# Optimization experiments

Hardware: AMD Instinct MI355X
Metric: run time of the kernel (lower is better)

Reference implementation:

```python
import jax, jax.numpy as jnp
import numpy as np

jax.config.update("jax_enable_x64", True)  # exact int64 fixed-point requantization

QMIN, QMAX = 0, 255  # 8-bit asymmetric activations


def _mul_m0_shift(acc, M0, shift):
    """gemmlowp-style fixed-point rescale: round((acc*M0)>>31) >> shift (rounding)."""
    prod = acc.astype(jnp.int64) * M0.astype(jnp.int64)
    nudge = jnp.where(prod >= 0, jnp.int64(1 << 30), jnp.int64(1 - (1 << 30)))
    hi = (prod + nudge) >> 31  # rounding-doubling high mul
    sh = shift.astype(jnp.int64)
    return (hi + (jnp.int64(1) << (sh - 1))) >> sh  # rounding right shift


def _requant(acc, M0, shift, z_out):
    return jnp.clip(_mul_m0_shift(acc, M0, shift) + z_out, QMIN, QMAX).astype(jnp.int32)


def _qconv(q, w, z_in, M0, shift, z_out, pad):
    # int8-style conv: subtract input zero-point, integer accumulate (exact in fp32
    # since |acc| < 2^24 by construction), then fixed-point requantize.
    xf = (q - z_in).astype(jnp.float32)
    acc = jax.lax.conv_general_dilated(
        xf, w, (1, 1), [(pad, pad), (pad, pad)],
        dimension_numbers=("NCHW", "OIHW", "NCHW"))
    return _requant(jnp.round(acc).astype(jnp.int64), M0, shift, z_out)


def _qbn(q, z_in, w, b, M0, shift, z_out):
    # fused quantized BN: per-channel integer affine + fixed-point requantize
    acc = (q.astype(jnp.int64) - z_in) * w.astype(jnp.int64)[None, :, None, None] \
          + b.astype(jnp.int64)[None, :, None, None]
    return _requant(acc, M0, shift, z_out)


def setup_inputs() -> dict:
    key = jax.random.key(0)
    ks = jax.random.split(key, 10)
    B, Cin, H, W = 32, 256, 56, 56
    width, Cout = 64, 256
    x = jax.random.randint(ks[0], (B, Cin, H, W), 0, 256, dtype=jnp.int32)
    w1 = jax.random.randint(ks[1], (width, Cin, 1, 1), -63, 64).astype(jnp.float32)
    w2 = jax.random.randint(ks[2], (width, width, 3, 3), -63, 64).astype(jnp.float32)
    w3 = jax.random.randint(ks[3], (Cout, width, 1, 1), -63, 64).astype(jnp.float32)
    bn1_w = jax.random.randint(ks[4], (width,), 100, 160).astype(jnp.float32)
    bn1_b = jax.random.randint(ks[5], (width,), -1000, 1000).astype(jnp.float32)
    bn2_w = jax.random.randint(ks[6], (width,), 100, 160).astype(jnp.float32)
    bn2_b = jax.random.randint(ks[7], (width,), -1000, 1000).astype(jnp.float32)
    bn3_w = jax.random.randint(ks[8], (Cout,), 100, 160).astype(jnp.float32)
    bn3_b = jax.random.randint(ks[9], (Cout,), -1000, 1000).astype(jnp.float32)
    conv_zin = jnp.array([128, 128, 128], jnp.int32)
    conv_m0 = jnp.array([1518500250] * 3, jnp.int32)
    conv_shift = jnp.array([9, 9, 9], jnp.int32)
    conv_zout = jnp.array([128, 128, 128], jnp.int32)
    bn_m0 = jnp.array([1073741824] * 3, jnp.int32)
    bn_shift = jnp.array([6, 6, 6], jnp.int32)
    bn_zout = jnp.array([128, 128, 128], jnp.int32)
    add_z = jnp.array([128, 128], jnp.int32)
    add_m0 = jnp.array([1073741824] * 2, jnp.int32)
    add_shift = jnp.array([1, 1], jnp.int32)
    add_zout = jnp.array(128, jnp.int32)
    return dict(x=x, w1=w1, w2=w2, w3=w3,
                bn1_w=bn1_w, bn1_b=bn1_b, bn2_w=bn2_w, bn2_b=bn2_b,
                bn3_w=bn3_w, bn3_b=bn3_b,
                conv_zin=conv_zin, conv_m0=conv_m0, conv_shift=conv_shift,
                conv_zout=conv_zout, bn_m0=bn_m0, bn_shift=bn_shift,
                bn_zout=bn_zout, add_z=add_z, add_m0=add_m0,
                add_shift=add_shift, add_zout=add_zout)


def reference(x, w1, w2, w3, bn1_w, bn1_b, bn2_w, bn2_b, bn3_w, bn3_b,
              conv_zin, conv_m0, conv_shift, conv_zout,
              bn_m0, bn_shift, bn_zout,
              add_z, add_m0, add_shift, add_zout):
    identity = x  # a_bit == target_bit -> rescale_matrix path skipped, conv_x = x
    out = _qconv(x, w1, conv_zin[0], conv_m0[0], conv_shift[0], conv_zout[0], 0)
    out = _qbn(out, conv_zout[0], bn1_w, bn1_b, bn_m0[0], bn_shift[0], bn_zout[0])
    out = _qconv(out, w2, conv_zin[1], conv_m0[1], conv_shift[1], conv_zout[1], 1)
    out = _qbn(out, conv_zout[1], bn2_w, bn2_b, bn_m0[1], bn_shift[1], bn_zout[1])
    out = _qconv(out, w3, conv_zin[2], conv_m0[2], conv_shift[2], conv_zout[2], 0)
    out = _qbn(out, conv_zout[2], bn3_w, bn3_b, bn_m0[2], bn_shift[2], bn_zout[2])
    # QuantizedAdd: rescale both branches to the output scale, add, clamp
    ra = _mul_m0_shift(identity.astype(jnp.int64) - add_z[0], add_m0[0], add_shift[0])
    rb = _mul_m0_shift(out.astype(jnp.int64) - add_z[1], add_m0[1], add_shift[1])
    return jnp.clip(ra + rb + add_zout, QMIN, QMAX).astype(jnp.int32)
```

## Files before the change

### kernel.cpp

```cpp
#include <hip/hip_runtime.h>


typedef int v4i __attribute__((ext_vector_type(4)));

#define BATCH 32
#define CIN 256
#define CMID 64
#define HW 3136
#define W56 56

__device__ __forceinline__ int requant_q(int acc, int M0, int shift, int zout) {
    long long prod = (long long)acc * (long long)M0;
    long long nudge = (prod >= 0) ? (1LL << 30) : (1LL - (1LL << 30));
    long long hi = (prod + nudge) >> 31;
    long long r = (hi + (1LL << (shift - 1))) >> shift;
    int v = (int)r + zout;
    return v < 0 ? 0 : (v > 255 ? 255 : v);
}

__device__ __forceinline__ long long mulshift_ll(long long v, int M0, int shift) {
    long long prod = v * (long long)M0;
    long long nudge = (prod >= 0) ? (1LL << 30) : (1LL - (1LL << 30));
    long long hi = (prod + nudge) >> 31;
    return (hi + (1LL << (shift - 1))) >> shift;
}

__device__ __forceinline__ v4i pack16f(const float* src, int stride) {
    v4i r;
#pragma unroll
    for (int d = 0; d < 4; ++d) {
        unsigned int u = 0;
#pragma unroll
        for (int by = 0; by < 4; ++by) {
            int v = (int)src[(d * 4 + by) * stride];
            u |= ((unsigned int)(v & 255)) << (8 * by);
        }
        r[d] = (int)u;
    }
    return r;
}

__global__ __launch_bounds__(256) void k_conv1(
    const int* __restrict__ x, const float* __restrict__ w1,
    const float* __restrict__ bn_w, const float* __restrict__ bn_b,
    const int* __restrict__ conv_zin, const int* __restrict__ conv_m0,
    const int* __restrict__ conv_shift, const int* __restrict__ conv_zout,
    const int* __restrict__ bn_m0, const int* __restrict__ bn_shift,
    const int* __restrict__ bn_zout, signed char* __restrict__ t1)
{
    __shared__ v4i sm[640];
    const int tid = threadIdx.x, lane = tid & 63, wv = tid >> 6;
    const int col = lane & 15, koff = lane >> 4;
    const int nbase = blockIdx.x * 128;
    const int co0 = wv * 16;

    v4i a[4];
#pragma unroll
    for (int ks = 0; ks < 4; ++ks)
        a[ks] = pack16f(w1 + (size_t)(co0 + col) * 256 + ks * 64 + koff * 16, 1);

    const int p = tid & 127, ch = tid >> 7;
    const int np = nbase + p;
    const int pb = np / HW, phw = np - pb * HW;
    const int zin = conv_zin[0];

    v4i acc[8];
#pragma unroll
    for (int i = 0; i < 8; ++i) acc[i] = (v4i){0, 0, 0, 0};

    for (int ks = 0; ks < 4; ++ks) {
        unsigned int pk[8];
        const size_t xb = ((size_t)pb * CIN + ks * 64 + ch * 32) * HW + phw;
#pragma unroll
        for (int d = 0; d < 8; ++d) {
            unsigned int u = 0;
#pragma unroll
            for (int by = 0; by < 4; ++by) {
                int v = x[xb + (size_t)(d * 4 + by) * HW] - zin;
                u |= ((unsigned int)(v & 255)) << (8 * by);
            }
            pk[d] = u;
        }
        __syncthreads();
        v4i* dst = &sm[p * 5 + ch * 2];
        v4i w0, w1v;
        w0[0] = (int)pk[0]; w0[1] = (int)pk[1]; w0[2] = (int)pk[2]; w0[3] = (int)pk[3];
        w1v[0] = (int)pk[4]; w1v[1] = (int)pk[5]; w1v[2] = (int)pk[6]; w1v[3] = (int)pk[7];
        dst[0] = w0; dst[1] = w1v;
        __syncthreads();
#pragma unroll
        for (int nt = 0; nt < 8; ++nt) {
            v4i bf = sm[(nt * 16 + col) * 5 + koff];
            acc[nt] = __builtin_amdgcn_mfma_i32_16x16x64_i8(a[ks], bf, acc[nt], 0, 0, 0);
        }
    }

    const int cm0 = conv_m0[0], csh = conv_shift[0], czo = conv_zout[0];
    const int bm0 = bn_m0[0], bsh = bn_shift[0], bzo = bn_zout[0];
    const int zin2 = conv_zin[1];
    const int rowb = koff * 4;
    int bw[4], bb[4];
#pragma unroll
    for (int r = 0; r < 4; ++r) {
        bw[r] = (int)bn_w[co0 + rowb + r];
        bb[r] = (int)bn_b[co0 + rowb + r];
    }
#pragma unroll
    for (int nt = 0; nt < 8; ++nt) {
        int n = nbase + nt * 16 + col;
        unsigned int pkd = 0;
#pragma unroll
        for (int r = 0; r < 4; ++r) {
            int q = requant_q(acc[nt][r], cm0, csh, czo);
            int a2 = (q - czo) * bw[r] + bb[r];
            int q2 = requant_q(a2, bm0, bsh, bzo);
            pkd |= ((unsigned int)((q2 - zin2) & 255)) << (8 * r);
        }
        *(unsigned int*)(t1 + (size_t)n * 64 + co0 + rowb) = pkd;
    }
}

__global__ __launch_bounds__(256) void k_conv2(
    const signed char* __restrict__ t1, const float* __restrict__ w2,
    const float* __restrict__ bn_w, const float* __restrict__ bn_b,
    const int* __restrict__ conv_zin, const int* __restrict__ conv_m0,
    const int* __restrict__ conv_shift, const int* __restrict__ conv_zout,
    const int* __restrict__ bn_m0, const int* __restrict__ bn_shift,
    const int* __restrict__ bn_zout, signed char* __restrict__ t2)
{
    __shared__ v4i sm[1120];
    const int tid = threadIdx.x, lane = tid & 63, wv = tid >> 6;
    const int col = lane & 15, koff = lane >> 4;
    const int b = blockIdx.y;
    const int r0 = blockIdx.x * 2;
    const int co0 = wv * 16;

    v4i a[9];
#pragma unroll
    for (int t = 0; t < 9; ++t)
        a[t] = pack16f(w2 + ((size_t)(co0 + col) * 64 + koff * 16) * 9 + t, 9);

    const v4i* t1v = (const v4i*)t1;
#pragma unroll
    for (int k = 0; k < 4; ++k) {
        int idx = tid + k * 256;
        if (idx < 896) {
            int pixl = idx >> 2, part = idx & 3;
            int lrow = pixl / W56, gw = pixl - lrow * W56;
            int grow = r0 - 1 + lrow;
            v4i v = (v4i){0, 0, 0, 0};
            if ((unsigned)grow < 56u)
                v = t1v[(size_t)(b * HW + grow * W56 + gw) * 4 + part];
            sm[pixl * 5 + part] = v;
        }
    }
    __syncthreads();

    v4i acc[7];
#pragma unroll
    for (int i = 0; i < 7; ++i) acc[i] = (v4i){0, 0, 0, 0};

#pragma unroll
    for (int kh = 0; kh < 3; ++kh) {
#pragma unroll
        for (int kw = 0; kw < 3; ++kw) {
            v4i af = a[kh * 3 + kw];
#pragma unroll
            for (int nt = 0; nt < 7; ++nt) {
                int pix = nt * 16 + col;
                int orow = pix >= W56 ? 1 : 0;
                int wc = pix - orow * W56;
                int sr = orow + kh;
                int sw = wc + kw - 1;
                bool valid = (unsigned)sw < 56u;
                v4i bf = sm[(sr * W56 + (valid ? sw : 0)) * 5 + koff];
                if (!valid) { bf[0] = 0; bf[1] = 0; bf[2] = 0; bf[3] = 0; }
                acc[nt] = __builtin_amdgcn_mfma_i32_16x16x64_i8(af, bf, acc[nt], 0, 0, 0);
            }
        }
    }

    const int cm0 = conv_m0[1], csh = conv_shift[1], czo = conv_zout[1];
    const int bm0 = bn_m0[1], bsh = bn_shift[1], bzo = bn_zout[1];
    const int zin3 = conv_zin[2];
    const int rowb = koff * 4;
    int bw[4], bb[4];
#pragma unroll
    for (int r = 0; r < 4; ++r) {
        bw[r] = (int)bn_w[co0 + rowb + r];
        bb[r] = (int)bn_b[co0 + rowb + r];
    }
#pragma unroll
    for (int nt = 0; nt < 7; ++nt) {
        int pix = nt * 16 + col;
        int n = b * HW + r0 * W56 + pix;
        unsigned int pkd = 0;
#pragma unroll
        for (int r = 0; r < 4; ++r) {
            int q = requant_q(acc[nt][r], cm0, csh, czo);
            int a2 = (q - czo) * bw[r] + bb[r];
            int q2 = requant_q(a2, bm0, bsh, bzo);
            pkd |= ((unsigned int)((q2 - zin3) & 255)) << (8 * r);
        }
        *(unsigned int*)(t2 + (size_t)n * 64 + co0 + rowb) = pkd;
    }
}

__global__ __launch_bounds__(256) void k_conv3(
    const signed char* __restrict__ t2, const float* __restrict__ w3,
    const float* __restrict__ bn_w, const float* __restrict__ bn_b,
    const int* __restrict__ x,
    const int* __restrict__ conv_m0, const int* __restrict__ conv_shift,
    const int* __restrict__ conv_zout,
    const int* __restrict__ bn_m0, const int* __restrict__ bn_shift,
    const int* __restrict__ bn_zout,
    const int* __restrict__ add_z, const int* __restrict__ add_m0,
    const int* __restrict__ add_shift, const int* __restrict__ add_zout,
    int* __restrict__ out)
{
    __shared__ v4i sm[640];
    const int tid = threadIdx.x, lane = tid & 63, wv = tid >> 6;
    const int col = lane & 15, koff = lane >> 4;
    const int nbase = blockIdx.x * 128;
    const int co0 = blockIdx.y * 64 + wv * 16;

    v4i a = pack16f(w3 + (size_t)(co0 + col) * 64 + koff * 16, 1);

    const v4i* t2v = (const v4i*)t2;
#pragma unroll
    for (int k = 0; k < 2; ++k) {
        int idx = tid + k * 256;
        int pixl = idx >> 2, part = idx & 3;
        sm[pixl * 5 + part] = t2v[(size_t)(nbase + pixl) * 4 + part];
    }
    __syncthreads();

    v4i acc[8];
#pragma unroll
    for (int i = 0; i < 8; ++i) acc[i] = (v4i){0, 0, 0, 0};
#pragma unroll
    for (int nt = 0; nt < 8; ++nt) {
        v4i bf = sm[(nt * 16 + col) * 5 + koff];
        acc[nt] = __builtin_amdgcn_mfma_i32_16x16x64_i8(a, bf, acc[nt], 0, 0, 0);
    }

    const int cm0 = conv_m0[2], csh = conv_shift[2], czo = conv_zout[2];
    const int bm0 = bn_m0[2], bsh = bn_shift[2], bzo = bn_zout[2];
    const int az0 = add_z[0], az1 = add_z[1];
    const int am0 = add_m0[0], am1 = add_m0[1];
    const int ash0 = add_shift[0], ash1 = add_shift[1];
    const int azout = add_zout[0];
    const int rowb = koff * 4;
    int bw[4], bb[4];
#pragma unroll
    for (int r = 0; r < 4; ++r) {
        bw[r] = (int)bn_w[co0 + rowb + r];
        bb[r] = (int)bn_b[co0 + rowb + r];
    }
#pragma unroll
    for (int nt = 0; nt < 8; ++nt) {
        int n = nbase + nt * 16 + col;
        int pb = n / HW, phw = n - pb * HW;
#pragma unroll
        for (int r = 0; r < 4; ++r) {
            int co = co0 + rowb + r;
            int q = requant_q(acc[nt][r], cm0, csh, czo);
            int a2 = (q - czo) * bw[r] + bb[r];
            int q2 = requant_q(a2, bm0, bsh, bzo);
            size_t ix = ((size_t)pb * CIN + co) * HW + phw;
            int idv = x[ix];
            long long ra = mulshift_ll((long long)(idv - az0), am0, ash0);
            long long rb = mulshift_ll((long long)(q2 - az1), am1, ash1);
            int res = (int)(ra + rb) + azout;
            res = res < 0 ? 0 : (res > 255 ? 255 : res);
            out[ix] = res;
        }
    }
}

extern "C" void kernel_launch(void* const* d_in, const int* in_sizes, int n_in,
                              void* d_out, int out_size, void* d_ws, size_t ws_size,
                              hipStream_t stream) {
    const int* x = (const int*)d_in[0];
    const float* w1 = (const float*)d_in[1];
    const float* w2 = (const float*)d_in[2];
    const float* w3 = (const float*)d_in[3];
    const float* bn1_w = (const float*)d_in[4];
    const float* bn1_b = (const float*)d_in[5];
    const float* bn2_w = (const float*)d_in[6];
    const float* bn2_b = (const float*)d_in[7];
    const float* bn3_w = (const float*)d_in[8];
    const float* bn3_b = (const float*)d_in[9];
    const int* conv_zin = (const int*)d_in[10];
    const int* conv_m0 = (const int*)d_in[11];
    const int* conv_shift = (const int*)d_in[12];
    const int* conv_zout = (const int*)d_in[13];
    const int* bn_m0 = (const int*)d_in[14];
    const int* bn_shift = (const int*)d_in[15];
    const int* bn_zout = (const int*)d_in[16];
    const int* add_z = (const int*)d_in[17];
    const int* add_m0 = (const int*)d_in[18];
    const int* add_shift = (const int*)d_in[19];
    const int* add_zout = (const int*)d_in[20];

    signed char* t1 = (signed char*)d_ws;
    signed char* t2 = t1 + (size_t)BATCH * HW * CMID;

    k_conv1<<<dim3(784), dim3(256), 0, stream>>>(x, w1, bn1_w, bn1_b,
        conv_zin, conv_m0, conv_shift, conv_zout, bn_m0, bn_shift, bn_zout, t1);
    k_conv2<<<dim3(28, 32), dim3(256), 0, stream>>>(t1, w2, bn2_w, bn2_b,
        conv_zin, conv_m0, conv_shift, conv_zout, bn_m0, bn_shift, bn_zout, t2);
    k_conv3<<<dim3(784, 4), dim3(256), 0, stream>>>(t2, w3, bn3_w, bn3_b, x,
        conv_m0, conv_shift, conv_zout, bn_m0, bn_shift, bn_zout,
        add_z, add_m0, add_shift, add_zout, (int*)d_out);
}
```

Before: 286.9 us.

## Precompute int8 residual in conv1, prepack weights, prefetch x, enlarge conv2 tile

While conv1 reads x, it now also computes the rescaled identity branch and stores it as int8. conv3 then reads one byte per element instead of re-reading the int32 input, which cuts the largest DRAM stream. A small prep kernel packs all three weight tensors into MFMA fragment layout once, replacing the per-block float-to-int8 packing. conv1 also prefetches the next K-slice of x into registers while the MFMAs run, and conv2 processes 4 rows per block with precomputed pixel coordinates. The risks are that the int8 residual store truncates values if the rescaled identity does not fit in a signed byte, and that the extra register pressure in conv1 and conv2 may lower occupancy.

```diff
diff --git a/kernel.cpp b/kernel.cpp
--- a/kernel.cpp
+++ b/kernel.cpp
@@ -8,6 +8,11 @@
 #define CMID 64
 #define HW 3136
 #define W56 56
+
+#define T1_BYTES ((size_t)BATCH * HW * CMID)
+#define RA_BYTES ((size_t)BATCH * HW * CIN)
+#define WP_BYTES ((size_t)68 * 64 * 16)
+#define NEED_FULL (WP_BYTES + 2 * T1_BYTES + RA_BYTES)
 
 __device__ __forceinline__ int requant_q(int acc, int M0, int shift, int zout) {
     long long prod = (long long)acc * (long long)M0;
@@ -40,13 +45,43 @@
     return r;
 }
 
+__global__ __launch_bounds__(256) void k_prep(
+    const float* __restrict__ w1, const float* __restrict__ w2,
+    const float* __restrict__ w3, v4i* __restrict__ wp)
+{
+    int id = blockIdx.x * 256 + threadIdx.x;
+    int fid = id >> 6, lane = id & 63;
+    if (fid >= 68) return;
+    int col = lane & 15, ci0 = (lane >> 4) * 16;
+    const float* src;
+    int stride;
+    if (fid < 16) {
+        int wv = fid >> 2, ks = fid & 3;
+        src = w1 + (size_t)(wv * 16 + col) * 256 + ks * 64 + ci0;
+        stride = 1;
+    } else if (fid < 52) {
+        int i = fid - 16, wv = i / 9, t = i - wv * 9;
+        src = w2 + ((size_t)(wv * 16 + col) * 64 + ci0) * 9 + t;
+        stride = 9;
+    } else {
+        int s = fid - 52;
+        src = w3 + (size_t)(s * 16 + col) * 64 + ci0;
+        stride = 1;
+    }
+    wp[fid * 64 + lane] = pack16f(src, stride);
+}
+
 __global__ __launch_bounds__(256) void k_conv1(
-    const int* __restrict__ x, const float* __restrict__ w1,
+    const int* __restrict__ x, const v4i* __restrict__ wp1,
     const float* __restrict__ bn_w, const float* __restrict__ bn_b,
     const int* __restrict__ conv_zin, const int* __restrict__ conv_m0,
     const int* __restrict__ conv_shift, const int* __restrict__ conv_zout,
     const int* __restrict__ bn_m0, const int* __restrict__ bn_shift,
-    const int* __restrict__ bn_zout, signed char* __restrict__ t1)
+    const int* __restrict__ bn_zout,
+    const int* __restrict__ add_z, const int* __restrict__ add_m0,
+    const int* __restrict__ add_shift,
+    signed char* __restrict__ ra8, const int use_ra,
+    signed char* __restrict__ t1)
 {
     __shared__ v4i sm[640];
     const int tid = threadIdx.x, lane = tid & 63, wv = tid >> 6;
@@ -56,42 +91,68 @@
 
     v4i a[4];
 #pragma unroll
-    for (int ks = 0; ks < 4; ++ks)
-        a[ks] = pack16f(w1 + (size_t)(co0 + col) * 256 + ks * 64 + koff * 16, 1);
+    for (int ks = 0; ks < 4; ++ks) a[ks] = wp1[(wv * 4 + ks) * 64 + lane];
 
     const int p = tid & 127, ch = tid >> 7;
     const int np = nbase + p;
     const int pb = np / HW, phw = np - pb * HW;
     const int zin = conv_zin[0];
-
-    v4i acc[8];
-#pragma unroll
-    for (int i = 0; i < 8; ++i) acc[i] = (v4i){0, 0, 0, 0};
-
-    for (int ks = 0; ks < 4; ++ks) {
-        unsigned int pk[8];
-        const size_t xb = ((size_t)pb * CIN + ks * 64 + ch * 32) * HW + phw;
+    const int az0 = add_z[0], am0 = add_m0[0], ash0 = add_shift[0];
+
+    unsigned int pk[8], pk2[8];
+    {
+        const size_t xb = ((size_t)pb * CIN + ch * 32) * HW + phw;
 #pragma unroll
         for (int d = 0; d < 8; ++d) {
             unsigned int u = 0;
 #pragma unroll
             for (int by = 0; by < 4; ++by) {
-                int v = x[xb + (size_t)(d * 4 + by) * HW] - zin;
-                u |= ((unsigned int)(v & 255)) << (8 * by);
+                size_t ix = xb + (size_t)(d * 4 + by) * HW;
+                int v = x[ix];
+                if (use_ra)
+                    ra8[ix] = (signed char)(int)mulshift_ll((long long)(v - az0), am0, ash0);
+                u |= ((unsigned int)((v - zin) & 255)) << (8 * by);
             }
             pk[d] = u;
         }
+    }
+
+    v4i acc[8];
+#pragma unroll
+    for (int i = 0; i < 8; ++i) acc[i] = (v4i){0, 0, 0, 0};
+
+    for (int ks = 0; ks < 4; ++ks) {
         __syncthreads();
         v4i* dst = &sm[p * 5 + ch * 2];
-        v4i w0, w1v;
-        w0[0] = (int)pk[0]; w0[1] = (int)pk[1]; w0[2] = (int)pk[2]; w0[3] = (int)pk[3];
+        v4i w0v, w1v;
+        w0v[0] = (int)pk[0]; w0v[1] = (int)pk[1]; w0v[2] = (int)pk[2]; w0v[3] = (int)pk[3];
         w1v[0] = (int)pk[4]; w1v[1] = (int)pk[5]; w1v[2] = (int)pk[6]; w1v[3] = (int)pk[7];
-        dst[0] = w0; dst[1] = w1v;
+        dst[0] = w0v; dst[1] = w1v;
         __syncthreads();
+        if (ks < 3) {
+            const size_t xb = ((size_t)pb * CIN + (ks + 1) * 64 + ch * 32) * HW + phw;
+#pragma unroll
+            for (int d = 0; d < 8; ++d) {
+                unsigned int u = 0;
+#pragma unroll
+                for (int by = 0; by < 4; ++by) {
+                    size_t ix = xb + (size_t)(d * 4 + by) * HW;
+                    int v = x[ix];
+                    if (use_ra)
+                        ra8[ix] = (signed char)(int)mulshift_ll((long long)(v - az0), am0, ash0);
+                    u |= ((unsigned int)((v - zin) & 255)) << (8 * by);
+                }
+                pk2[d] = u;
+            }
+        }
 #pragma unroll
         for (int nt = 0; nt < 8; ++nt) {
             v4i bf = sm[(nt * 16 + col) * 5 + koff];
             acc[nt] = __builtin_amdgcn_mfma_i32_16x16x64_i8(a[ks], bf, acc[nt], 0, 0, 0);
+        }
+        if (ks < 3) {
+#pragma unroll
+            for (int d = 0; d < 8; ++d) pk[d] = pk2[d];
         }
     }
 
@@ -121,44 +182,51 @@
 }
 
 __global__ __launch_bounds__(256) void k_conv2(
-    const signed char* __restrict__ t1, const float* __restrict__ w2,
+    const signed char* __restrict__ t1, const v4i* __restrict__ wp2,
     const float* __restrict__ bn_w, const float* __restrict__ bn_b,
     const int* __restrict__ conv_zin, const int* __restrict__ conv_m0,
     const int* __restrict__ conv_shift, const int* __restrict__ conv_zout,
     const int* __restrict__ bn_m0, const int* __restrict__ bn_shift,
     const int* __restrict__ bn_zout, signed char* __restrict__ t2)
 {
-    __shared__ v4i sm[1120];
+    __shared__ v4i sm[1680];
     const int tid = threadIdx.x, lane = tid & 63, wv = tid >> 6;
     const int col = lane & 15, koff = lane >> 4;
     const int b = blockIdx.y;
-    const int r0 = blockIdx.x * 2;
+    const int r0 = blockIdx.x * 4;
     const int co0 = wv * 16;
 
     v4i a[9];
 #pragma unroll
-    for (int t = 0; t < 9; ++t)
-        a[t] = pack16f(w2 + ((size_t)(co0 + col) * 64 + koff * 16) * 9 + t, 9);
+    for (int t = 0; t < 9; ++t) a[t] = wp2[(wv * 9 + t) * 64 + lane];
 
     const v4i* t1v = (const v4i*)t1;
 #pragma unroll
-    for (int k = 0; k < 4; ++k) {
+    for (int k = 0; k < 6; ++k) {
         int idx = tid + k * 256;
-        if (idx < 896) {
+        if (idx < 1344) {
             int pixl = idx >> 2, part = idx & 3;
             int lrow = pixl / W56, gw = pixl - lrow * W56;
             int grow = r0 - 1 + lrow;
             v4i v = (v4i){0, 0, 0, 0};
             if ((unsigned)grow < 56u)
-                v = t1v[(size_t)(b * HW + grow * W56 + gw) * 4 + part];
+                v = t1v[((size_t)b * HW + grow * W56 + gw) * 4 + part];
             sm[pixl * 5 + part] = v;
         }
     }
     __syncthreads();
 
-    v4i acc[7];
-#pragma unroll
-    for (int i = 0; i < 7; ++i) acc[i] = (v4i){0, 0, 0, 0};
+    int orow[14], wc[14];
+#pragma unroll
+    for (int nt = 0; nt < 14; ++nt) {
+        int pix = nt * 16 + col;
+        orow[nt] = pix / W56;
+        wc[nt] = pix - orow[nt] * W56;
+    }
+
+    v4i acc[14];
+#pragma unroll
+    for (int i = 0; i < 14; ++i) acc[i] = (v4i){0, 0, 0, 0};
 
 #pragma unroll
     for (int kh = 0; kh < 3; ++kh) {
@@ -166,12 +234,9 @@
         for (int kw = 0; kw < 3; ++kw) {
             v4i af = a[kh * 3 + kw];
 #pragma unroll
-            for (int nt = 0; nt < 7; ++nt) {
-                int pix = nt * 16 + col;
-                int orow = pix >= W56 ? 1 : 0;
-                int wc = pix - orow * W56;
-                int sr = orow + kh;
-                int sw = wc + kw - 1;
+            for (int nt = 0; nt < 14; ++nt) {
+                int sr = orow[nt] + kh;
+                int sw = wc[nt] + kw - 1;
                 bool valid = (unsigned)sw < 56u;
                 v4i bf = sm[(sr * W56 + (valid ? sw : 0)) * 5 + koff];
                 if (!valid) { bf[0] = 0; bf[1] = 0; bf[2] = 0; bf[3] = 0; }
@@ -191,7 +256,7 @@
         bb[r] = (int)bn_b[co0 + rowb + r];
     }
 #pragma unroll
-    for (int nt = 0; nt < 7; ++nt) {
+    for (int nt = 0; nt < 14; ++nt) {
         int pix = nt * 16 + col;
         int n = b * HW + r0 * W56 + pix;
         unsigned int pkd = 0;
@@ -207,9 +272,9 @@
 }
 
 __global__ __launch_bounds__(256) void k_conv3(
-    const signed char* __restrict__ t2, const float* __restrict__ w3,
+    const signed char* __restrict__ t2, const v4i* __restrict__ wp3,
     const float* __restrict__ bn_w, const float* __restrict__ bn_b,
-    const int* __restrict__ x,
+    const int* __restrict__ x, const signed char* __restrict__ ra8, const int use_ra,
     const int* __restrict__ conv_m0, const int* __restrict__ conv_shift,
     const int* __restrict__ conv_zout,
     const int* __restrict__ bn_m0, const int* __restrict__ bn_shift,
@@ -224,7 +289,7 @@
     const int nbase = blockIdx.x * 128;
     const int co0 = blockIdx.y * 64 + wv * 16;
 
-    v4i a = pack16f(w3 + (size_t)(co0 + col) * 64 + koff * 16, 1);
+    v4i a = wp3[(blockIdx.y * 4 + wv) * 64 + lane];
 
     const v4i* t2v = (const v4i*)t2;
 #pragma unroll
@@ -268,10 +333,11 @@
             int a2 = (q - czo) * bw[r] + bb[r];
             int q2 = requant_q(a2, bm0, bsh, bzo);
             size_t ix = ((size_t)pb * CIN + co) * HW + phw;
-            int idv = x[ix];
-            long long ra = mulshift_ll((long long)(idv - az0), am0, ash0);
+            int rav;
+            if (use_ra) rav = (int)ra8[ix];
+            else rav = (int)mulshift_ll((long long)(x[ix] - az0), am0, ash0);
             long long rb = mulshift_ll((long long)(q2 - az1), am1, ash1);
-            int res = (int)(ra + rb) + azout;
+            int res = rav + (int)rb + azout;
             res = res < 0 ? 0 : (res > 255 ? 255 : res);
             out[ix] = res;
         }
@@ -303,14 +369,23 @@
     const int* add_shift = (const int*)d_in[19];
     const int* add_zout = (const int*)d_in[20];
 
-    signed char* t1 = (signed char*)d_ws;
-    signed char* t2 = t1 + (size_t)BATCH * HW * CMID;
-
-    k_conv1<<<dim3(784), dim3(256), 0, stream>>>(x, w1, bn1_w, bn1_b,
-        conv_zin, conv_m0, conv_shift, conv_zout, bn_m0, bn_shift, bn_zout, t1);
-    k_conv2<<<dim3(28, 32), dim3(256), 0, stream>>>(t1, w2, bn2_w, bn2_b,
+    v4i* wp = (v4i*)d_ws;
+    signed char* t1 = (signed char*)d_ws + WP_BYTES;
+    signed char* t2 = t1 + T1_BYTES;
+    signed char* ra8 = t2 + T1_BYTES;
+    const int use_ra = (ws_size >= NEED_FULL) ? 1 : 0;
+
+    const v4i* wp1 = wp;
+    const v4i* wp2 = wp + 16 * 64;
+    const v4i* wp3 = wp + 52 * 64;
+
+    k_prep<<<dim3(17), dim3(256), 0, stream>>>(w1, w2, w3, wp);
+    k_conv1<<<dim3(784), dim3(256), 0, stream>>>(x, wp1, bn1_w, bn1_b,
+        conv_zin, conv_m0, conv_shift, conv_zout, bn_m0, bn_shift, bn_zout,
+        add_z, add_m0, add_shift, ra8, use_ra, t1);
+    k_conv2<<<dim3(14, 32), dim3(256), 0, stream>>>(t1, wp2, bn2_w, bn2_b,
         conv_zin, conv_m0, conv_shift, conv_zout, bn_m0, bn_shift, bn_zout, t2);
-    k_conv3<<<dim3(784, 4), dim3(256), 0, stream>>>(t2, w3, bn3_w, bn3_b, x,
-        conv_m0, conv_shift, conv_zout, bn_m0, bn_shift, bn_zout,
+    k_conv3<<<dim3(784, 4), dim3(256), 0, stream>>>(t2, wp3, bn3_w, bn3_b,
+        x, ra8, use_ra, conv_m0, conv_shift, conv_zout, bn_m0, bn_shift, bn_zout,
         add_z, add_m0, add_shift, add_zout, (int*)d_out);
 }
```

Measured after the change: 347.7 us. +21.2%, slower.
